# Kernel tuning notes

Hardware: AMD Instinct MI355X
Metric: run time of the kernel (lower is better)

## Reference

```python
import jax, jax.numpy as jnp
import numpy as np

TEMP = 0.07
HARD_K = 512
EMB_D = 768
PROJ_D = 128
QUEUE = 32768
BATCH = 2048
NUM_CLASSES = 2


def setup_inputs() -> dict:
    key = jax.random.key(0)
    ks = jax.random.split(key, 8)
    embeddings = jax.random.normal(ks[0], (BATCH, EMB_D), dtype=jnp.float32)
    labels = jax.random.randint(ks[1], (BATCH,), 0, NUM_CLASSES)
    # projector params: Linear(D,D) -> ReLU -> Linear(D,128)
    W1 = jax.random.normal(ks[2], (EMB_D, EMB_D), dtype=jnp.float32) * 0.02
    b1 = jnp.zeros((EMB_D,), dtype=jnp.float32)
    W2 = jax.random.normal(ks[3], (EMB_D, PROJ_D), dtype=jnp.float32) * 0.02
    b2 = jnp.zeros((PROJ_D,), dtype=jnp.float32)
    # queue buffers: L2-normalized random embeddings (as in __init__) with valid labels
    qe = jax.random.normal(ks[4], (QUEUE, PROJ_D), dtype=jnp.float32)
    queue_embeddings = qe / jnp.linalg.norm(qe, axis=1, keepdims=True)
    queue_labels = jax.random.randint(ks[5], (QUEUE,), 0, NUM_CLASSES)
    return {
        'embeddings': embeddings, 'labels': labels,
        'W1': W1, 'b1': b1, 'W2': W2, 'b2': b2,
        'queue_embeddings': queue_embeddings, 'queue_labels': queue_labels,
    }


def reference(embeddings, labels, W1, b1, W2, b2, queue_embeddings, queue_labels):
    n = embeddings.shape[0]
    # projector + L2 normalize
    h = jax.nn.relu(embeddings @ W1 + b1)
    z = h @ W2 + b2
    z = z / jnp.linalg.norm(z, axis=1, keepdims=True)  # (N, 128)

    # pairwise in-batch similarities, scaled by temperature
    S = (z @ z.T) / TEMP  # (N, N)
    same = labels[:, None] == labels[None, :]
    eye = jnp.eye(n, dtype=bool)
    pos_mask = same & ~eye           # positives: same label, not self
    neg_mask = ~same                 # in-batch negatives: different label

    # logsumexp over in-batch negatives per anchor (-inf rows -> -inf, handled by logaddexp)
    neg_batch = jnp.where(neg_mask, S, -jnp.inf)
    lse_batch = jax.scipy.special.logsumexp(neg_batch, axis=1)  # (N,)

    # hard negatives from queue: opposite-label, top-K by similarity
    sims_q = z @ queue_embeddings.T  # (N, Q)
    opp = (queue_labels[None, :] != labels[:, None]) & (queue_labels[None, :] >= 0)
    masked_q = jnp.where(opp, sims_q, -jnp.inf)
    topk_vals, _ = jax.lax.top_k(masked_q, HARD_K)  # (N, K); -inf pads drop from logsumexp
    # fallback (no opposite-label entries): first K queue embeddings regardless of label
    fallback = sims_q[:, :HARD_K]
    has_opp = opp.any(axis=1, keepdims=True)
    neg_q = jnp.where(has_opp, topk_vals, fallback) / TEMP
    lse_queue = jax.scipy.special.logsumexp(neg_q, axis=1)  # (N,)

    # all negatives for anchor i: batch negatives ++ queue hard negatives
    lse_neg = jnp.logaddexp(lse_batch, lse_queue)  # (N,)

    # per positive pair (i, j): log_prob = pos_sim - logsumexp([pos_sim, negs])
    log_prob = S - jnp.logaddexp(S, lse_neg[:, None])  # (N, N)
    losses = jnp.where(pos_mask, -log_prob, 0.0)
    count = pos_mask.sum()
    return jnp.where(count > 0, losses.sum() / count.astype(losses.dtype), 0.0)
```

## Files before the change

### kernel.cpp

```cpp
#include <hip/hip_runtime.h>
#include <hip/hip_fp16.h>

#define BATCH_N   2048
#define EMB_D_    768
#define PROJ_D_   128
#define QUEUE_N   32768
#define HARD_K_   512
static constexpr float INV_T  = 1.0f / 0.07f;
static constexpr float WLO    = 0.12f;
static constexpr float S8ENC  = 255.0f / 0.88f;
static constexpr float BINW   = 0.88f / 255.0f;

typedef __attribute__((ext_vector_type(8))) short short8;
typedef __attribute__((ext_vector_type(4))) short short4v;
typedef __attribute__((ext_vector_type(4))) float f32x4;

__device__ __forceinline__ unsigned short f2bf(float f) {
    unsigned u = __float_as_uint(f);
    unsigned r = u + 0x7fffu + ((u >> 16) & 1u);
    return (unsigned short)(r >> 16);
}
__device__ __forceinline__ float bf2f(short s) {
    return __uint_as_float(((unsigned)(unsigned short)s) << 16);
}
__device__ __forceinline__ int opp_of(int mylab, const int* __restrict__ qcnt) {
    const int same = (mylab == 0) ? qcnt[0] : ((mylab == 1) ? qcnt[1] : 0);
    return qcnt[2] - same;
}

__global__ void __launch_bounds__(256) mfma_nt_plain(const short* __restrict__ Ab,
                                                     const short* __restrict__ Bb,
                                                     float* __restrict__ C, int N) {
    __shared__ __align__(16) short As[128 * 128];
    __shared__ __align__(16) short Bs[128 * 128];
    const int t = threadIdx.x;
    const int lane = t & 63, wv = t >> 6;
    const int l16 = lane & 15, l4 = lane >> 4;
    const int m0 = blockIdx.y * 128, n0 = blockIdx.x * 128;

    #pragma unroll
    for (int it = 0; it < 8; ++it) {
        const int r = it * 4 + wv, row = r * 4 + l4, cg = l16 ^ (row & 15);
        __builtin_amdgcn_global_load_lds(
            (const __attribute__((address_space(1))) void*)(Ab + (size_t)(m0 + row) * 128 + cg * 8),
            (__attribute__((address_space(3))) void*)(As + r * 512), 16, 0, 0);
    }
    #pragma unroll
    for (int it = 0; it < 8; ++it) {
        const int r = it * 4 + wv, row = r * 4 + l4, cg = l16 ^ (row & 15);
        __builtin_amdgcn_global_load_lds(
            (const __attribute__((address_space(1))) void*)(Bb + (size_t)(n0 + row) * 128 + cg * 8),
            (__attribute__((address_space(3))) void*)(Bs + r * 512), 16, 0, 0);
    }
    __syncthreads();

    const int wm = (wv & 1) * 64, wn = (wv >> 1) * 64;
    f32x4 acc[4][4];
    #pragma unroll
    for (int i = 0; i < 4; ++i)
        #pragma unroll
        for (int j = 0; j < 4; ++j) acc[i][j] = f32x4{0.f, 0.f, 0.f, 0.f};

    #pragma unroll
    for (int ks = 0; ks < 4; ++ks) {
        short8 af[4], bfr[4];
        const int ch = (ks * 4 + l4) ^ l16;
        #pragma unroll
        for (int i = 0; i < 4; ++i) {
            af[i]  = *(const short8*)(As + (wm + i * 16 + l16) * 128 + ch * 8);
            bfr[i] = *(const short8*)(Bs + (wn + i * 16 + l16) * 128 + ch * 8);
        }
        #pragma unroll
        for (int i = 0; i < 4; ++i)
            #pragma unroll
            for (int j = 0; j < 4; ++j)
                acc[i][j] = __builtin_amdgcn_mfma_f32_16x16x32_bf16(af[i], bfr[j], acc[i][j], 0, 0, 0);
    }
    #pragma unroll
    for (int i = 0; i < 4; ++i)
        #pragma unroll
        for (int r = 0; r < 4; ++r) {
            const int m = m0 + wm + i * 16 + l4 * 4 + r;
            #pragma unroll
            for (int j = 0; j < 4; ++j)
                C[(size_t)m * N + n0 + wn + j * 16 + l16] = acc[i][j][r];
        }
}

__global__ void __launch_bounds__(256) mfma_mask8(const short* __restrict__ Ab,
                                                  const short* __restrict__ Bb,
                                                  unsigned char* __restrict__ codes,
                                                  const int* __restrict__ labA,
                                                  const int* __restrict__ labB) {
    __shared__ __align__(16) short As[128 * 128];
    __shared__ __align__(16) short Bs[128 * 128];
    const int t = threadIdx.x;
    const int lane = t & 63, wv = t >> 6;
    const int l16 = lane & 15, l4 = lane >> 4;
    const int m0 = blockIdx.y * 128, n0 = blockIdx.x * 128;

    #pragma unroll
    for (int it = 0; it < 8; ++it) {
        const int r = it * 4 + wv, row = r * 4 + l4, cg = l16 ^ (row & 15);
        __builtin_amdgcn_global_load_lds(
            (const __attribute__((address_space(1))) void*)(Ab + (size_t)(m0 + row) * 128 + cg * 8),
            (__attribute__((address_space(3))) void*)(As + r * 512), 16, 0, 0);
    }
    #pragma unroll
    for (int it = 0; it < 8; ++it) {
        const int r = it * 4 + wv, row = r * 4 + l4, cg = l16 ^ (row & 15);
        __builtin_amdgcn_global_load_lds(
            (const __attribute__((address_space(1))) void*)(Bb + (size_t)(n0 + row) * 128 + cg * 8),
            (__attribute__((address_space(3))) void*)(Bs + r * 512), 16, 0, 0);
    }
    __syncthreads();

    const int wm = (wv & 1) * 64, wn = (wv >> 1) * 64;
    f32x4 acc[4][4];
    #pragma unroll
    for (int i = 0; i < 4; ++i)
        #pragma unroll
        for (int j = 0; j < 4; ++j) acc[i][j] = f32x4{0.f, 0.f, 0.f, 0.f};

    #pragma unroll
    for (int ks = 0; ks < 4; ++ks) {
        short8 af[4], bfr[4];
        const int ch = (ks * 4 + l4) ^ l16;
        #pragma unroll
        for (int i = 0; i < 4; ++i) {
            af[i]  = *(const short8*)(As + (wm + i * 16 + l16) * 128 + ch * 8);
            bfr[i] = *(const short8*)(Bs + (wn + i * 16 + l16) * 128 + ch * 8);
        }
        #pragma unroll
        for (int i = 0; i < 4; ++i)
            #pragma unroll
            for (int j = 0; j < 4; ++j)
                acc[i][j] = __builtin_amdgcn_mfma_f32_16x16x32_bf16(af[i], bfr[j], acc[i][j], 0, 0, 0);
    }

    const float C0 = 1.0f - WLO * S8ENC;
    float a0[4], a1[4];
    #pragma unroll
    for (int j = 0; j < 4; ++j) {
        const int q = labB[n0 + wn + j * 16 + l16];
        a0[j] = (q >= 0 && q != 0) ? C0 : -1e9f;
        a1[j] = (q >= 0 && q != 1) ? C0 : -1e9f;
    }
    int la[16];
    #pragma unroll
    for (int i = 0; i < 4; ++i)
        #pragma unroll
        for (int r = 0; r < 4; ++r)
            la[i * 4 + r] = labA[m0 + wm + i * 16 + l4 * 4 + r];

    #pragma unroll
    for (int i = 0; i < 4; ++i) {
        #pragma unroll
        for (int r = 0; r < 4; ++r) {
            const int m  = m0 + wm + i * 16 + l4 * 4 + r;
            const bool z = (la[i * 4 + r] == 0);
            unsigned pk = 0;
            #pragma unroll
            for (int j = 0; j < 4; ++j) {
                const float add = z ? a0[j] : a1[j];
                const float f = fmaf(acc[i][j][r], S8ENC, add);
#if __has_builtin(__builtin_amdgcn_cvt_pk_u8_f32)
                pk = __builtin_amdgcn_cvt_pk_u8_f32(f, j, pk);
#else
                const unsigned c = (unsigned)fminf(fmaxf(f, 0.0f), 255.0f);
                pk |= c << (8 * j);
#endif
            }
            *(unsigned*)(codes + (size_t)m * QUEUE_N + n0 + wn + l16 * 4) = pk;
        }
    }
}

template<typename OutT, bool RELU>
__global__ void __launch_bounds__(256) mfma_nt_k(const short* __restrict__ Ab,
                                                 const short* __restrict__ Bb,
                                                 const float* __restrict__ bias,
                                                 OutT* __restrict__ C,
                                                 int N, int K) {
    __shared__ __align__(16) short As[128 * 128];
    __shared__ __align__(16) short Bs[128 * 128];
    const int t = threadIdx.x;
    const int lane = t & 63, wv = t >> 6;
    const int l16 = lane & 15, l4 = lane >> 4;
    const int m0 = blockIdx.y * 128, n0 = blockIdx.x * 128;
    const int wm = (wv & 1) * 64, wn = (wv >> 1) * 64;

    f32x4 acc[4][4];
    #pragma unroll
    for (int i = 0; i < 4; ++i)
        #pragma unroll
        for (int j = 0; j < 4; ++j) acc[i][j] = f32x4{0.f, 0.f, 0.f, 0.f};

    for (int kb = 0; kb < K; kb += 128) {
        __syncthreads();
        #pragma unroll
        for (int it = 0; it < 8; ++it) {
            const int r = it * 4 + wv, row = r * 4 + l4, cg = l16 ^ (row & 15);
            __builtin_amdgcn_global_load_lds(
                (const __attribute__((address_space(1))) void*)(Ab + (size_t)(m0 + row) * K + kb + cg * 8),
                (__attribute__((address_space(3))) void*)(As + r * 512), 16, 0, 0);
        }
        #pragma unroll
        for (int it = 0; it < 8; ++it) {
            const int r = it * 4 + wv, row = r * 4 + l4, cg = l16 ^ (row & 15);
            __builtin_amdgcn_global_load_lds(
                (const __attribute__((address_space(1))) void*)(Bb + (size_t)(n0 + row) * K + kb + cg * 8),
                (__attribute__((address_space(3))) void*)(Bs + r * 512), 16, 0, 0);
        }
        __syncthreads();
        #pragma unroll
        for (int ks = 0; ks < 4; ++ks) {
            short8 af[4], bfr[4];
            const int ch = (ks * 4 + l4) ^ l16;
            #pragma unroll
            for (int i = 0; i < 4; ++i) {
                af[i]  = *(const short8*)(As + (wm + i * 16 + l16) * 128 + ch * 8);
                bfr[i] = *(const short8*)(Bs + (wn + i * 16 + l16) * 128 + ch * 8);
            }
            #pragma unroll
            for (int i = 0; i < 4; ++i)
                #pragma unroll
                for (int j = 0; j < 4; ++j)
                    acc[i][j] = __builtin_amdgcn_mfma_f32_16x16x32_bf16(af[i], bfr[j], acc[i][j], 0, 0, 0);
        }
    }

    float bsv[4];
    #pragma unroll
    for (int j = 0; j < 4; ++j) bsv[j] = bias[n0 + wn + j * 16 + l16];
    #pragma unroll
    for (int i = 0; i < 4; ++i)
        #pragma unroll
        for (int r = 0; r < 4; ++r) {
            const int m = m0 + wm + i * 16 + l4 * 4 + r;
            #pragma unroll
            for (int j = 0; j < 4; ++j) {
                const int n = n0 + wn + j * 16 + l16;
                float v = acc[i][j][r] + bsv[j];
                if (RELU) v = fmaxf(v, 0.0f);
                if constexpr (sizeof(OutT) == 2) ((short*)C)[(size_t)m * N + n] = (short)f2bf(v);
                else                             ((float*)C)[(size_t)m * N + n] = v;
            }
        }
}

__global__ void __launch_bounds__(256) mfma_z_norm(const short* __restrict__ Ab,
                                                   const short* __restrict__ Bb,
                                                   const float* __restrict__ bias,
                                                   short* __restrict__ zb) {
    __shared__ __align__(16) short As[128 * 128];
    __shared__ __align__(16) short Bs[128 * 128];
    __shared__ float ssq[128];
    const int t = threadIdx.x;
    const int lane = t & 63, wv = t >> 6;
    const int l16 = lane & 15, l4 = lane >> 4;
    const int m0 = blockIdx.x * 128;
    const int wm = (wv & 1) * 64, wn = (wv >> 1) * 64;
    const int K = EMB_D_;

    if (t < 128) ssq[t] = 0.0f;

    f32x4 acc[4][4];
    #pragma unroll
    for (int i = 0; i < 4; ++i)
        #pragma unroll
        for (int j = 0; j < 4; ++j) acc[i][j] = f32x4{0.f, 0.f, 0.f, 0.f};

    for (int kb = 0; kb < K; kb += 128) {
        __syncthreads();
        #pragma unroll
        for (int it = 0; it < 8; ++it) {
            const int r = it * 4 + wv, row = r * 4 + l4, cg = l16 ^ (row & 15);
            __builtin_amdgcn_global_load_lds(
                (const __attribute__((address_space(1))) void*)(Ab + (size_t)(m0 + row) * K + kb + cg * 8),
                (__attribute__((address_space(3))) void*)(As + r * 512), 16, 0, 0);
        }
        #pragma unroll
        for (int it = 0; it < 8; ++it) {
            const int r = it * 4 + wv, row = r * 4 + l4, cg = l16 ^ (row & 15);
            __builtin_amdgcn_global_load_lds(
                (const __attribute__((address_space(1))) void*)(Bb + (size_t)(row) * K + kb + cg * 8),
                (__attribute__((address_space(3))) void*)(Bs + r * 512), 16, 0, 0);
        }
        __syncthreads();
        #pragma unroll
        for (int ks = 0; ks < 4; ++ks) {
            short8 af[4], bfr[4];
            const int ch = (ks * 4 + l4) ^ l16;
            #pragma unroll
            for (int i = 0; i < 4; ++i) {
                af[i]  = *(const short8*)(As + (wm + i * 16 + l16) * 128 + ch * 8);
                bfr[i] = *(const short8*)(Bs + (wn + i * 16 + l16) * 128 + ch * 8);
            }
            #pragma unroll
            for (int i = 0; i < 4; ++i)
                #pragma unroll
                for (int j = 0; j < 4; ++j)
                    acc[i][j] = __builtin_amdgcn_mfma_f32_16x16x32_bf16(af[i], bfr[j], acc[i][j], 0, 0, 0);
        }
    }

    float bsv[4];
    #pragma unroll
    for (int j = 0; j < 4; ++j) bsv[j] = bias[wn + j * 16 + l16];
    #pragma unroll
    for (int i = 0; i < 4; ++i)
        #pragma unroll
        for (int r = 0; r < 4; ++r) {
            float p = 0.0f;
            #pragma unroll
            for (int j = 0; j < 4; ++j) {
                acc[i][j][r] += bsv[j];
                p += acc[i][j][r] * acc[i][j][r];
            }
            #pragma unroll
            for (int o = 8; o > 0; o >>= 1) p += __shfl_xor(p, o);
            if (l16 == 0) atomicAdd(&ssq[wm + i * 16 + l4 * 4 + r], p);
        }
    __syncthreads();
    #pragma unroll
    for (int i = 0; i < 4; ++i)
        #pragma unroll
        for (int r = 0; r < 4; ++r) {
            const int lrow = wm + i * 16 + l4 * 4 + r;
            const float inv = rsqrtf(ssq[lrow]);
            #pragma unroll
            for (int j = 0; j < 4; ++j)
                zb[(size_t)(m0 + lrow) * PROJ_D_ + wn + j * 16 + l16] =
                    (short)f2bf(acc[i][j][r] * inv);
        }
}

__global__ void __launch_bounds__(256) prep(const float* __restrict__ emb, short* __restrict__ embb,
                                            const float* __restrict__ queue, short* __restrict__ qb,
                                            const int* __restrict__ qlab, int* __restrict__ qcnt,
                                            const float* __restrict__ W1, short* __restrict__ w1t,
                                            const float* __restrict__ W2, short* __restrict__ w2t) {
    __shared__ float tile[64][65];
    const int b = blockIdx.x, t = threadIdx.x;
    if (b < 1536) {
        const int i = b * 256 + t;
        const float4 f = ((const float4*)emb)[i];
        short4v o = {(short)f2bf(f.x), (short)f2bf(f.y), (short)f2bf(f.z), (short)f2bf(f.w)};
        ((short4v*)embb)[i] = o;
    } else if (b < 5632) {
        const int i = (b - 1536) * 256 + t;
        const float4 f = ((const float4*)queue)[i];
        short4v o = {(short)f2bf(f.x), (short)f2bf(f.y), (short)f2bf(f.z), (short)f2bf(f.w)};
        ((short4v*)qb)[i] = o;
    } else if (b < 5664) {
        const int i = (b - 5632) * 256 + t;
        int c0 = 0, c1 = 0, cv = 0;
        for (int j = i; j < QUEUE_N; j += 8192) {
            const int q = qlab[j];
            c0 += (q == 0); c1 += (q == 1); cv += (q >= 0);
        }
        #pragma unroll
        for (int o = 32; o > 0; o >>= 1) {
            c0 += __shfl_xor(c0, o); c1 += __shfl_xor(c1, o); cv += __shfl_xor(cv, o);
        }
        if ((t & 63) == 0) {
            atomicAdd(&qcnt[0], c0); atomicAdd(&qcnt[1], c1); atomicAdd(&qcnt[2], cv);
        }
    } else {
        const int bid = b - 5664;
        const float* A; short* At; int R, C, bx, by;
        if (bid < 144) { A = W1; At = w1t; R = EMB_D_; C = EMB_D_;  bx = (bid % 12) * 64; by = (bid / 12) * 64; }
        else { const int b2 = bid - 144; A = W2; At = w2t; R = EMB_D_; C = PROJ_D_; bx = (b2 & 1) * 64; by = (b2 >> 1) * 64; }
        const int tc = t & 63, tg = t >> 6;
        #pragma unroll
        for (int i = 0; i < 16; i++) {
            const int r = tg * 16 + i;
            tile[r][tc] = A[(size_t)(by + r) * C + bx + tc];
        }
        __syncthreads();
        #pragma unroll
        for (int i = 0; i < 16; i++) {
            const int r = tg * 16 + i;
            At[(size_t)(bx + r) * R + by + tc] = (short)f2bf(tile[tc][r]);
        }
    }
}

__global__ void __launch_bounds__(256) topk_lse_u8(const unsigned char* __restrict__ codes,
                                                   const int* __restrict__ qcnt,
                                                   const int* __restrict__ labels,
                                                   float* __restrict__ lseq,
                                                   int* __restrict__ flag) {
    const int row = blockIdx.x, t = threadIdx.x;
    __shared__ int hist[256];
    __shared__ int suf[256];
    __shared__ int s_bin;
    __shared__ float scf[4];
    hist[t] = 0;
    __syncthreads();

    const uint4* rowp = (const uint4*)(codes + (size_t)row * QUEUE_N);
    #pragma unroll
    for (int k = 0; k < 8; k++) {
        const uint4 u = rowp[k * 256 + t];
        const unsigned w[4] = {u.x, u.y, u.z, u.w};
        #pragma unroll
        for (int q = 0; q < 4; q++)
            #pragma unroll
            for (int s = 0; s < 4; s++) {
                const int c = (w[q] >> (8 * s)) & 0xFF;
                if (c) atomicAdd(&hist[c], 1);
            }
    }
    __syncthreads();

    suf[t] = hist[t];
    __syncthreads();
    for (int off = 1; off < 256; off <<= 1) {
        int add = (t + off < 256) ? suf[t + off] : 0;
        __syncthreads();
        suf[t] += add;
        __syncthreads();
    }
    const int total = suf[1];
    const int opp   = opp_of(labels[row], qcnt);
    if (total < HARD_K_ || opp < HARD_K_) {
        if (t == 0) flag[row] = 0;
        return;
    }
    {
        const int above = (t < 255) ? suf[t + 1] : 0;
        if (suf[t] >= HARD_K_ && above < HARD_K_) s_bin = t;
    }
    __syncthreads();
    const int b = s_bin;

    float e = 0.0f;
    if (t > b && hist[t]) e = (float)hist[t] * __expf((WLO + ((float)t - 0.5f) * BINW - 1.0f) * INV_T);
    #pragma unroll
    for (int o = 32; o > 0; o >>= 1) e += __shfl_xor(e, o);
    if ((t & 63) == 0) scf[t >> 6] = e;
    __syncthreads();
    if (t == 0) {
        const float Eab  = scf[0] + scf[1] + scf[2] + scf[3];
        const int   cab  = (b < 255) ? suf[b + 1] : 0;
        const float ebin = __expf((WLO + ((float)b - 0.5f) * BINW - 1.0f) * INV_T);
        const float sadj = Eab + (float)(HARD_K_ - cab) * ebin;
        lseq[row] = INV_T + __logf(sadj);
        flag[row] = 1;
    }
}

__device__ __forceinline__ void find_crossing(int* hist, int* grp, int target,
                                              int* s_bin, int* s_chi) {
    const int t = threadIdx.x;
    const int b0 = hist[4*t], b1 = hist[4*t+1], b2 = hist[4*t+2], b3 = hist[4*t+3];
    grp[t] = b0 + b1 + b2 + b3;
    __syncthreads();
    for (int off = 1; off < 256; off <<= 1) {
        int add = (t + off < 256) ? grp[t + off] : 0;
        __syncthreads();
        grp[t] += add;
        __syncthreads();
    }
    int cab = (t < 255) ? grp[t + 1] : 0;
    const int hb[4] = {b0, b1, b2, b3};
    #pragma unroll
    for (int i = 3; i >= 0; i--) {
        const int h = hb[i];
        if (cab < target && cab + h >= target) { *s_bin = 4*t + i; *s_chi = cab; }
        cab += h;
    }
    __syncthreads();
}

#define FOR_ALL_VALS(BODY)                                                   \
    _Pragma("unroll")                                                        \
    for (int _k = 0; _k < 64; _k++) {                                        \
        const float2 _f = __half22float2(*(const __half2*)&dv[_k]);          \
        { const float v = _f.x; BODY }                                       \
        { const float v = _f.y; BODY }                                       \
    }

__global__ void __launch_bounds__(256) topk_lse_fallback(const short* __restrict__ zb,
                                                         const short* __restrict__ qb,
                                                         const int* __restrict__ labels,
                                                         const int* __restrict__ qlab,
                                                         const int* __restrict__ qcnt,
                                                         const int* __restrict__ flag,
                                                         float* __restrict__ lseq) {
    const int row = blockIdx.x, t = threadIdx.x;
    if (flag[row]) return;
    const int opp = opp_of(labels[row], qcnt);

    __shared__ float zrow[128];
    __shared__ int hist[1024];
    __shared__ int grp[256];
    __shared__ int s_bin, s_chi, s_bin2, s_chi2;
    __shared__ float scf[4]; __shared__ int sci[4];
    if (t < 128) zrow[t] = bf2f(zb[(size_t)row * 128 + t]);
    __syncthreads();

    const int mylab = labels[row];
    unsigned dv[64];
    float rm = -1e30f, rs = 0.0f;
    for (int k = 0; k < 128; k++) {
        const int j = t + 256 * k;
        float d = 0.0f;
        #pragma unroll
        for (int c = 0; c < 16; ++c) {
            const short8 qv = *(const short8*)(qb + (size_t)j * 128 + c * 8);
            #pragma unroll
            for (int e = 0; e < 8; ++e) d += zrow[c * 8 + e] * bf2f(qv[e]);
        }
        if (j < HARD_K_) {
            const float sv = d * INV_T;
            if (sv > rm) { rs = rs * __expf(rm - sv) + 1.0f; rm = sv; }
            else         { rs += __expf(sv - rm); }
        }
        const int q = qlab[j];
        const float mv = (q != mylab && q >= 0) ? d : -65504.0f;
        const __half h = __float2half(mv);
        unsigned short* p = (unsigned short*)&dv[k >> 1];
        p[k & 1] = *(const unsigned short*)&h;
    }

    if (opp == 0) {
        #pragma unroll
        for (int o = 32; o > 0; o >>= 1) {
            const float om = __shfl_xor(rm, o), os = __shfl_xor(rs, o);
            const float nm = fmaxf(rm, om);
            rs = rs * __expf(rm - nm) + os * __expf(om - nm);
            rm = nm;
        }
        if ((t & 63) == 0) { scf[t >> 6] = rm; ((float*)sci)[t >> 6] = rs; }
        __syncthreads();
        if (t == 0) {
            float M = -1e30f, Sx = 0.0f;
            for (int w = 0; w < 4; w++) {
                const float nm = fmaxf(M, scf[w]);
                Sx = Sx * __expf(M - nm) + ((float*)sci)[w] * __expf(scf[w] - nm);
                M = nm;
            }
            lseq[row] = M + __logf(Sx);
        }
        return;
    }
    if (opp < HARD_K_) {
        float mm = -1e30f, ss = 0.0f;
        FOR_ALL_VALS(
            if (v > -60000.0f) {
                const float sv = v * INV_T;
                if (sv > mm) { ss = ss * __expf(mm - sv) + 1.0f; mm = sv; }
                else         { ss += __expf(sv - mm); }
            } )
        #pragma unroll
        for (int o = 32; o > 0; o >>= 1) {
            const float om = __shfl_xor(mm, o), os = __shfl_xor(ss, o);
            const float nm = fmaxf(mm, om);
            ss = ss * __expf(mm - nm) + os * __expf(om - nm);
            mm = nm;
        }
        if ((t & 63) == 0) { scf[t >> 6] = mm; ((float*)sci)[t >> 6] = ss; }
        __syncthreads();
        if (t == 0) {
            float M = -1e30f, Sx = 0.0f;
            for (int w = 0; w < 4; w++) {
                const float nm = fmaxf(M, scf[w]);
                Sx = Sx * __expf(M - nm) + ((float*)sci)[w] * __expf(scf[w] - nm);
                M = nm;
            }
            lseq[row] = M + __logf(Sx);
        }
        return;
    }

    float mloc = -1e30f;
    FOR_ALL_VALS( mloc = fmaxf(mloc, v); )
    #pragma unroll
    for (int o = 32; o > 0; o >>= 1) mloc = fmaxf(mloc, __shfl_xor(mloc, o));
    if ((t & 63) == 0) scf[t >> 6] = mloc;
    __syncthreads();
    const float m = fmaxf(fmaxf(scf[0], scf[1]), fmaxf(scf[2], scf[3]));

    int c1 = 0, c2 = 0;
    const float w1 = m - 0.25f, w2 = m - 1.0f;
    FOR_ALL_VALS( c1 += (v >= w1); c2 += (v >= w2); )
    #pragma unroll
    for (int o = 32; o > 0; o >>= 1) { c1 += __shfl_xor(c1, o); c2 += __shfl_xor(c2, o); }
    if ((t & 63) == 0) { sci[t >> 6] = c1; }
    __syncthreads();
    const int C1 = sci[0] + sci[1] + sci[2] + sci[3];
    __syncthreads();
    if ((t & 63) == 0) { sci[t >> 6] = c2; }
    __syncthreads();
    const int C2 = sci[0] + sci[1] + sci[2] + sci[3];

    float lo;
    if      (C1 >= HARD_K_) lo = w1;
    else if (C2 >= HARD_K_) lo = w2;
    else                    lo = -1.01f;
    const float range = m - lo;
    const float scale = 1024.0f / range;

    for (int k = t; k < 1024; k += 256) hist[k] = 0;
    __syncthreads();
    FOR_ALL_VALS(
        if (v >= lo) {
            const float bf = fminf((v - lo) * scale, 1023.0f);
            atomicAdd(&hist[(int)bf], 1);
        } )
    __syncthreads();
    find_crossing(hist, grp, HARD_K_, &s_bin, &s_chi);
    const int   bin1 = s_bin, chi1 = s_chi;
    const float binw = range * (1.0f / 1024.0f);
    const float lo1  = lo + bin1 * binw;
    const float ssc  = 1024.0f / binw;

    for (int k = t; k < 1024; k += 256) hist[k] = 0;
    __syncthreads();
    FOR_ALL_VALS(
        if (v >= lo) {
            const float bf = fminf((v - lo) * scale, 1023.0f);
            if ((int)bf == bin1) {
                const float sf = fminf(fmaxf((v - lo1) * ssc, 0.0f), 1023.0f);
                atomicAdd(&hist[(int)sf], 1);
            }
        } )
    __syncthreads();
    find_crossing(hist, grp, HARD_K_ - chi1, &s_bin2, &s_chi2);
    const float thr = lo1 + s_bin2 * (binw * (1.0f / 1024.0f));

    float sl = 0.0f; int cg = 0;
    FOR_ALL_VALS( if (v > thr) { cg++; sl += __expf((v - m) * INV_T); } )
    #pragma unroll
    for (int o = 32; o > 0; o >>= 1) { sl += __shfl_xor(sl, o); cg += __shfl_xor(cg, o); }
    if ((t & 63) == 0) { scf[t >> 6] = sl; sci[t >> 6] = cg; }
    __syncthreads();
    if (t == 0) {
        const float slt = scf[0] + scf[1] + scf[2] + scf[3];
        const int   cgt = sci[0] + sci[1] + sci[2] + sci[3];
        const float sadj = slt + ((float)HARD_K_ - (float)cgt) * __expf((thr - m) * INV_T);
        lseq[row] = m * INV_T + __logf(sadj);
    }
}

__global__ void __launch_bounds__(256) batch_row_loss(const float* __restrict__ S,
                                                      const int* __restrict__ labels,
                                                      const float* __restrict__ lse_queue,
                                                      float* __restrict__ part_out,
                                                      int* __restrict__ cnt_out) {
    const int t = threadIdx.x;
    const int wv = t >> 6, lane = t & 63;
    const int row = blockIdx.x * 4 + wv;
    __shared__ int lab[BATCH_N];
    for (int k = t; k < BATCH_N; k += 256) lab[k] = labels[k];
    __syncthreads();
    const int myLab = lab[row];
    const float4* rp4 = (const float4*)(S + (size_t)row * BATCH_N);
    const int4*   lb4 = (const int4*)lab;

    float v[32]; int lb[32];
    #pragma unroll
    for (int kk = 0; kk < 8; kk++) {
        const float4 f = rp4[lane + 64 * kk];
        const int4   l = lb4[lane + 64 * kk];
        v[4*kk+0] = f.x; v[4*kk+1] = f.y; v[4*kk+2] = f.z; v[4*kk+3] = f.w;
        lb[4*kk+0] = l.x; lb[4*kk+1] = l.y; lb[4*kk+2] = l.z; lb[4*kk+3] = l.w;
    }

    const float REF = INV_T;
    float sneg = 0.0f;
    #pragma unroll
    for (int k = 0; k < 32; k++) {
        const float ev = __expf(v[k] * INV_T - REF);
        sneg += (lb[k] != myLab) ? ev : 0.0f;
    }
    #pragma unroll
    for (int o = 32; o > 0; o >>= 1) sneg += __shfl_xor(sneg, o);
    const float lseb = (sneg > 0.0f) ? REF + __logf(sneg) : -1e30f;
    const float Lq = lse_queue[row];
    const float mx0 = fmaxf(lseb, Lq), mn0 = fminf(lseb, Lq);
    const float L = mx0 + __logf(1.0f + __expf(mn0 - mx0));

    float part = 0.0f; int cnt = 0;
    #pragma unroll
    for (int k = 0; k < 32; k++) {
        const int j = (lane + 64 * (k >> 2)) * 4 + (k & 3);
        if (lb[k] == myLab && j != row) {
            const float sv = v[k] * INV_T;
            const float mx = fmaxf(sv, L), mn = fminf(sv, L);
            part += (mx - sv) + __logf(1.0f + __expf(mn - mx));
            cnt++;
        }
    }
    #pragma unroll
    for (int o = 32; o > 0; o >>= 1) { part += __shfl_xor(part, o); cnt += __shfl_xor(cnt, o); }
    if (lane == 0) { part_out[row] = part; cnt_out[row] = cnt; }
}

__global__ void __launch_bounds__(256) finalize_loss(const float* __restrict__ part,
                                                     const int* __restrict__ cnt,
                                                     float* __restrict__ out) {
    const int t = threadIdx.x;
    float s = 0.0f; int c = 0;
    #pragma unroll
    for (int k = 0; k < 8; k++) { s += part[t + 256 * k]; c += cnt[t + 256 * k]; }
    #pragma unroll
    for (int o = 32; o > 0; o >>= 1) { s += __shfl_xor(s, o); c += __shfl_xor(c, o); }
    __shared__ float sf[4]; __shared__ int sc[4];
    if ((t & 63) == 0) { sf[t >> 6] = s; sc[t >> 6] = c; }
    __syncthreads();
    if (t == 0) {
        const float st = sf[0] + sf[1] + sf[2] + sf[3];
        const int   ct = sc[0] + sc[1] + sc[2] + sc[3];
        out[0] = (ct > 0) ? (st / (float)ct) : 0.0f;
    }
}

extern "C" void kernel_launch(void* const* d_in, const int* in_sizes, int n_in,
                              void* d_out, int out_size, void* d_ws, size_t ws_size,
                              hipStream_t stream) {
    const float* emb    = (const float*)d_in[0];
    const int*   labels = (const int*)  d_in[1];
    const float* W1     = (const float*)d_in[2];
    const float* b1     = (const float*)d_in[3];
    const float* W2     = (const float*)d_in[4];
    const float* b2     = (const float*)d_in[5];
    const float* queue  = (const float*)d_in[6];
    const int*   qlab   = (const int*)  d_in[7];

    char* ws = (char*)d_ws;
    float*         Sbuf  = (float*)        (ws);
    unsigned char* codes = (unsigned char*)(ws + 16777216);
    short*         embb  = (short*)        (ws + 83886080);
    short*         hbf   = (short*)        (ws + 87031808);
    short*         zb    = (short*)        (ws + 90177536);
    short*         qb    = (short*)        (ws + 90701824);
    short*         w1t   = (short*)        (ws + 99090432);
    short*         w2t   = (short*)        (ws + 100270080);
    float*         lseq  = (float*)        (ws + 100466688);
    int*           flag  = (int*)          (ws + 100474880);
    int*           qcnt  = (int*)          (ws + 100483072);
    float*         partb = (float*)        (ws + 100483136);
    int*           cntb  = (int*)          (ws + 100491328);

    hipMemsetAsync(ws + 100474880, 0, 8192 + 64, stream);

    dim3 blk(256);
    prep<<<dim3(5832), blk, 0, stream>>>(emb, embb, queue, qb, qlab, qcnt, W1, w1t, W2, w2t);
    mfma_nt_k<short, true><<<dim3(EMB_D_ / 128, BATCH_N / 128), blk, 0, stream>>>(embb, w1t, b1, hbf, EMB_D_, EMB_D_);
    mfma_z_norm<<<dim3(BATCH_N / 128), blk, 0, stream>>>(hbf, w2t, b2, zb);
    mfma_mask8<<<dim3(QUEUE_N / 128, BATCH_N / 128), blk, 0, stream>>>(zb, qb, codes, labels, qlab);
    topk_lse_u8<<<BATCH_N, blk, 0, stream>>>(codes, qcnt, labels, lseq, flag);
    topk_lse_fallback<<<BATCH_N, blk, 0, stream>>>(zb, qb, labels, qlab, qcnt, flag, lseq);
    mfma_nt_plain<<<dim3(BATCH_N / 128, BATCH_N / 128), blk, 0, stream>>>(zb, zb, Sbuf, BATCH_N);
    batch_row_loss<<<BATCH_N / 4, blk, 0, stream>>>(Sbuf, labels, lseq, partb, cntb);
    finalize_loss<<<1, blk, 0, stream>>>(partb, cntb, (float*)d_out);
}
```

Measured before the change: 181.4 us.

## Store in-batch similarity matrix as bf16 and double N-tiles per mask8 block

The in-batch similarity GEMM now writes a permuted bf16 matrix instead of fp32, packing four columns per 8-byte store. The row-loss kernel reads half the bytes and undoes the permutation through a permuted label table in shared memory. Separately, mfma_mask8 now covers two queue column tiles per block, reusing the A tile and prefetching the second B tile while the first tile's codes are written. The cost is bf16 rounding of the similarities before they are scaled by 1/T, plus halved grid parallelism in mask8.

```diff
diff --git a/kernel.cpp b/kernel.cpp
--- a/kernel.cpp
+++ b/kernel.cpp
@@ -28,9 +28,9 @@
     return qcnt[2] - same;
 }
 
-__global__ void __launch_bounds__(256) mfma_nt_plain(const short* __restrict__ Ab,
-                                                     const short* __restrict__ Bb,
-                                                     float* __restrict__ C, int N) {
+__global__ void __launch_bounds__(256) mfma_s_pack(const short* __restrict__ Ab,
+                                                   const short* __restrict__ Bb,
+                                                   short* __restrict__ C, int N) {
     __shared__ __align__(16) short As[128 * 128];
     __shared__ __align__(16) short Bs[128 * 128];
     const int t = threadIdx.x;
@@ -81,9 +81,10 @@
         #pragma unroll
         for (int r = 0; r < 4; ++r) {
             const int m = m0 + wm + i * 16 + l4 * 4 + r;
-            #pragma unroll
-            for (int j = 0; j < 4; ++j)
-                C[(size_t)m * N + n0 + wn + j * 16 + l16] = acc[i][j][r];
+            union { unsigned short u[4]; uint2 d; } pk;
+            #pragma unroll
+            for (int j = 0; j < 4; ++j) pk.u[j] = f2bf(acc[i][j][r]);
+            *(uint2*)(C + (size_t)m * N + n0 + wn + l16 * 4) = pk.d;
         }
 }
 
@@ -97,7 +98,8 @@
     const int t = threadIdx.x;
     const int lane = t & 63, wv = t >> 6;
     const int l16 = lane & 15, l4 = lane >> 4;
-    const int m0 = blockIdx.y * 128, n0 = blockIdx.x * 128;
+    const int m0 = blockIdx.y * 128;
+    const int wm = (wv & 1) * 64, wn = (wv >> 1) * 64;
 
     #pragma unroll
     for (int it = 0; it < 8; ++it) {
@@ -106,73 +108,93 @@
             (const __attribute__((address_space(1))) void*)(Ab + (size_t)(m0 + row) * 128 + cg * 8),
             (__attribute__((address_space(3))) void*)(As + r * 512), 16, 0, 0);
     }
-    #pragma unroll
-    for (int it = 0; it < 8; ++it) {
-        const int r = it * 4 + wv, row = r * 4 + l4, cg = l16 ^ (row & 15);
-        __builtin_amdgcn_global_load_lds(
-            (const __attribute__((address_space(1))) void*)(Bb + (size_t)(n0 + row) * 128 + cg * 8),
-            (__attribute__((address_space(3))) void*)(Bs + r * 512), 16, 0, 0);
-    }
-    __syncthreads();
-
-    const int wm = (wv & 1) * 64, wn = (wv >> 1) * 64;
-    f32x4 acc[4][4];
-    #pragma unroll
-    for (int i = 0; i < 4; ++i)
-        #pragma unroll
-        for (int j = 0; j < 4; ++j) acc[i][j] = f32x4{0.f, 0.f, 0.f, 0.f};
-
-    #pragma unroll
-    for (int ks = 0; ks < 4; ++ks) {
-        short8 af[4], bfr[4];
-        const int ch = (ks * 4 + l4) ^ l16;
-        #pragma unroll
-        for (int i = 0; i < 4; ++i) {
-            af[i]  = *(const short8*)(As + (wm + i * 16 + l16) * 128 + ch * 8);
-            bfr[i] = *(const short8*)(Bs + (wn + i * 16 + l16) * 128 + ch * 8);
-        }
-        #pragma unroll
-        for (int i = 0; i < 4; ++i)
-            #pragma unroll
-            for (int j = 0; j < 4; ++j)
-                acc[i][j] = __builtin_amdgcn_mfma_f32_16x16x32_bf16(af[i], bfr[j], acc[i][j], 0, 0, 0);
-    }
-
-    const float C0 = 1.0f - WLO * S8ENC;
-    float a0[4], a1[4];
-    #pragma unroll
-    for (int j = 0; j < 4; ++j) {
-        const int q = labB[n0 + wn + j * 16 + l16];
-        a0[j] = (q >= 0 && q != 0) ? C0 : -1e9f;
-        a1[j] = (q >= 0 && q != 1) ? C0 : -1e9f;
-    }
+    {
+        const int n0 = (blockIdx.x * 2) * 128;
+        #pragma unroll
+        for (int it = 0; it < 8; ++it) {
+            const int r = it * 4 + wv, row = r * 4 + l4, cg = l16 ^ (row & 15);
+            __builtin_amdgcn_global_load_lds(
+                (const __attribute__((address_space(1))) void*)(Bb + (size_t)(n0 + row) * 128 + cg * 8),
+                (__attribute__((address_space(3))) void*)(Bs + r * 512), 16, 0, 0);
+        }
+    }
+
     int la[16];
     #pragma unroll
     for (int i = 0; i < 4; ++i)
         #pragma unroll
         for (int r = 0; r < 4; ++r)
             la[i * 4 + r] = labA[m0 + wm + i * 16 + l4 * 4 + r];
-
-    #pragma unroll
-    for (int i = 0; i < 4; ++i) {
-        #pragma unroll
-        for (int r = 0; r < 4; ++r) {
-            const int m  = m0 + wm + i * 16 + l4 * 4 + r;
-            const bool z = (la[i * 4 + r] == 0);
-            unsigned pk = 0;
-            #pragma unroll
-            for (int j = 0; j < 4; ++j) {
-                const float add = z ? a0[j] : a1[j];
-                const float f = fmaf(acc[i][j][r], S8ENC, add);
+    const float C0 = 1.0f - WLO * S8ENC;
+    __syncthreads();
+
+    #pragma unroll
+    for (int tt = 0; tt < 2; ++tt) {
+        const int n0 = (blockIdx.x * 2 + tt) * 128;
+
+        f32x4 acc[4][4];
+        #pragma unroll
+        for (int i = 0; i < 4; ++i)
+            #pragma unroll
+            for (int j = 0; j < 4; ++j) acc[i][j] = f32x4{0.f, 0.f, 0.f, 0.f};
+
+        #pragma unroll
+        for (int ks = 0; ks < 4; ++ks) {
+            short8 af[4], bfr[4];
+            const int ch = (ks * 4 + l4) ^ l16;
+            #pragma unroll
+            for (int i = 0; i < 4; ++i) {
+                af[i]  = *(const short8*)(As + (wm + i * 16 + l16) * 128 + ch * 8);
+                bfr[i] = *(const short8*)(Bs + (wn + i * 16 + l16) * 128 + ch * 8);
+            }
+            #pragma unroll
+            for (int i = 0; i < 4; ++i)
+                #pragma unroll
+                for (int j = 0; j < 4; ++j)
+                    acc[i][j] = __builtin_amdgcn_mfma_f32_16x16x32_bf16(af[i], bfr[j], acc[i][j], 0, 0, 0);
+        }
+
+        if (tt == 0) {
+            __syncthreads();
+            const int n1 = (blockIdx.x * 2 + 1) * 128;
+            #pragma unroll
+            for (int it = 0; it < 8; ++it) {
+                const int r = it * 4 + wv, row = r * 4 + l4, cg = l16 ^ (row & 15);
+                __builtin_amdgcn_global_load_lds(
+                    (const __attribute__((address_space(1))) void*)(Bb + (size_t)(n1 + row) * 128 + cg * 8),
+                    (__attribute__((address_space(3))) void*)(Bs + r * 512), 16, 0, 0);
+            }
+        }
+
+        float a0[4], a1[4];
+        #pragma unroll
+        for (int j = 0; j < 4; ++j) {
+            const int q = labB[n0 + wn + j * 16 + l16];
+            a0[j] = (q >= 0 && q != 0) ? C0 : -1e9f;
+            a1[j] = (q >= 0 && q != 1) ? C0 : -1e9f;
+        }
+        #pragma unroll
+        for (int i = 0; i < 4; ++i) {
+            #pragma unroll
+            for (int r = 0; r < 4; ++r) {
+                const int m  = m0 + wm + i * 16 + l4 * 4 + r;
+                const bool z = (la[i * 4 + r] == 0);
+                unsigned pk = 0;
+                #pragma unroll
+                for (int j = 0; j < 4; ++j) {
+                    const float add = z ? a0[j] : a1[j];
+                    const float f = fmaf(acc[i][j][r], S8ENC, add);
 #if __has_builtin(__builtin_amdgcn_cvt_pk_u8_f32)
-                pk = __builtin_amdgcn_cvt_pk_u8_f32(f, j, pk);
+                    pk = __builtin_amdgcn_cvt_pk_u8_f32(f, j, pk);
 #else
-                const unsigned c = (unsigned)fminf(fmaxf(f, 0.0f), 255.0f);
-                pk |= c << (8 * j);
+                    const unsigned c = (unsigned)fminf(fmaxf(f, 0.0f), 255.0f);
+                    pk |= c << (8 * j);
 #endif
-            }
-            *(unsigned*)(codes + (size_t)m * QUEUE_N + n0 + wn + l16 * 4) = pk;
-        }
+                }
+                *(unsigned*)(codes + (size_t)m * QUEUE_N + n0 + wn + l16 * 4) = pk;
+            }
+        }
+        if (tt == 0) __syncthreads();
     }
 }
 
@@ -646,7 +668,7 @@
     }
 }
 
-__global__ void __launch_bounds__(256) batch_row_loss(const float* __restrict__ S,
+__global__ void __launch_bounds__(256) batch_row_loss(const short* __restrict__ S,
                                                       const int* __restrict__ labels,
                                                       const float* __restrict__ lse_queue,
                                                       float* __restrict__ part_out,
@@ -654,20 +676,28 @@
     const int t = threadIdx.x;
     const int wv = t >> 6, lane = t & 63;
     const int row = blockIdx.x * 4 + wv;
-    __shared__ int lab[BATCH_N];
-    for (int k = t; k < BATCH_N; k += 256) lab[k] = labels[k];
-    __syncthreads();
-    const int myLab = lab[row];
-    const float4* rp4 = (const float4*)(S + (size_t)row * BATCH_N);
-    const int4*   lb4 = (const int4*)lab;
+    __shared__ int plab[BATCH_N];
+    for (int idx = t; idx < BATCH_N; idx += 256) {
+        const int col = (idx & ~63) + ((idx & 3) << 4) + ((idx >> 2) & 15);
+        plab[idx] = labels[col];
+    }
+    __syncthreads();
+    const int myLab = labels[row];
+    const uint4* rp = (const uint4*)(S + (size_t)row * BATCH_N);
 
     float v[32]; int lb[32];
     #pragma unroll
-    for (int kk = 0; kk < 8; kk++) {
-        const float4 f = rp4[lane + 64 * kk];
-        const int4   l = lb4[lane + 64 * kk];
-        v[4*kk+0] = f.x; v[4*kk+1] = f.y; v[4*kk+2] = f.z; v[4*kk+3] = f.w;
-        lb[4*kk+0] = l.x; lb[4*kk+1] = l.y; lb[4*kk+2] = l.z; lb[4*kk+3] = l.w;
+    for (int kk = 0; kk < 4; kk++) {
+        const uint4 u = rp[lane + 64 * kk];
+        const unsigned w[4] = {u.x, u.y, u.z, u.w};
+        const int base = (lane + 64 * kk) * 8;
+        #pragma unroll
+        for (int q = 0; q < 4; q++) {
+            v[kk * 8 + 2 * q]     = __uint_as_float(w[q] << 16);
+            v[kk * 8 + 2 * q + 1] = __uint_as_float(w[q] & 0xFFFF0000u);
+            lb[kk * 8 + 2 * q]     = plab[base + 2 * q];
+            lb[kk * 8 + 2 * q + 1] = plab[base + 2 * q + 1];
+        }
     }
 
     const float REF = INV_T;
@@ -687,8 +717,9 @@
     float part = 0.0f; int cnt = 0;
     #pragma unroll
     for (int k = 0; k < 32; k++) {
-        const int j = (lane + 64 * (k >> 2)) * 4 + (k & 3);
-        if (lb[k] == myLab && j != row) {
+        const int idx = ((lane + 64 * (k >> 3)) * 8) + (k & 7);
+        const int col = (idx & ~63) + ((idx & 3) << 4) + ((idx >> 2) & 15);
+        if (lb[k] == myLab && col != row) {
             const float sv = v[k] * INV_T;
             const float mx = fmaxf(sv, L), mn = fminf(sv, L);
             part += (mx - sv) + __logf(1.0f + __expf(mn - mx));
@@ -732,7 +763,7 @@
     const int*   qlab   = (const int*)  d_in[7];
 
     char* ws = (char*)d_ws;
-    float*         Sbuf  = (float*)        (ws);
+    short*         Sbuf  = (short*)        (ws);
     unsigned char* codes = (unsigned char*)(ws + 16777216);
     short*         embb  = (short*)        (ws + 83886080);
     short*         hbf   = (short*)        (ws + 87031808);
@@ -752,10 +783,10 @@
     prep<<<dim3(5832), blk, 0, stream>>>(emb, embb, queue, qb, qlab, qcnt, W1, w1t, W2, w2t);
     mfma_nt_k<short, true><<<dim3(EMB_D_ / 128, BATCH_N / 128), blk, 0, stream>>>(embb, w1t, b1, hbf, EMB_D_, EMB_D_);
     mfma_z_norm<<<dim3(BATCH_N / 128), blk, 0, stream>>>(hbf, w2t, b2, zb);
-    mfma_mask8<<<dim3(QUEUE_N / 128, BATCH_N / 128), blk, 0, stream>>>(zb, qb, codes, labels, qlab);
+    mfma_mask8<<<dim3(QUEUE_N / 256, BATCH_N / 128), blk, 0, stream>>>(zb, qb, codes, labels, qlab);
     topk_lse_u8<<<BATCH_N, blk, 0, stream>>>(codes, qcnt, labels, lseq, flag);
     topk_lse_fallback<<<BATCH_N, blk, 0, stream>>>(zb, qb, labels, qlab, qcnt, flag, lseq);
-    mfma_nt_plain<<<dim3(BATCH_N / 128, BATCH_N / 128), blk, 0, stream>>>(zb, zb, Sbuf, BATCH_N);
+    mfma_s_pack<<<dim3(BATCH_N / 128, BATCH_N / 128), blk, 0, stream>>>(zb, zb, Sbuf, BATCH_N);
     batch_row_loss<<<BATCH_N / 4, blk, 0, stream>>>(Sbuf, labels, lseq, partb, cntb);
     finalize_loss<<<1, blk, 0, stream>>>(partb, cntb, (float*)d_out);
 }
```

After: 177.0 us. 1.02x faster.
